# Kernel tuning notes

Hardware: AMD Instinct MI355X
Metric: run time of the kernel (lower is better)

Reference implementation:

```python
import jax, jax.numpy as jnp
import numpy as np

EPS = 1e-5  # BatchNorm eps (PyTorch default)


def gcn_conv(x, edge_index, W, b):
    """PyG GCNConv with add_self_loops=True, normalize=True.
    out[j] = sum_{(i->j)} x_w[i] / sqrt(deg_i * deg_j) + x_w[j] / deg_j + b,
    deg_j = 1 + in-degree(j) (self-loop included)."""
    n = x.shape[0]
    src, dst = edge_index[0], edge_index[1]
    ones = jnp.ones(src.shape[0], x.dtype)
    deg = 1.0 + jax.ops.segment_sum(ones, dst, num_segments=n)  # [n]
    dis = jax.lax.rsqrt(deg)
    xw = x @ W  # [n, out]
    msg = xw[src] * (dis[src] * dis[dst])[:, None]  # gather + per-edge norm
    agg = jax.ops.segment_sum(msg, dst, num_segments=n)  # scatter-add
    agg = agg + xw * (1.0 / deg)[:, None]  # self-loop term
    return agg + b


def bn_relu(x, gamma, beta):
    # BatchNorm1d over the node dim (training-mode batch stats) + ReLU
    mean = x.mean(axis=0)
    var = x.var(axis=0)
    return jax.nn.relu((x - mean) * jax.lax.rsqrt(var + EPS) * gamma + beta)


def wireframe_gnn(x, edge_index, layers, fcW, fcb):
    feats = [x]
    h = x
    for (W, b, g, be) in layers:  # fixed small n_layers loop
        h = bn_relu(gcn_conv(h, edge_index, W, b), g, be)
        feats.append(h)
    cat = jnp.concatenate(feats, axis=1)
    return jax.nn.relu(cat @ fcW + fcb)


N_L, N_J = 50000, 25000
D_FC, NF = 1024, 256
E_L, E_J = 400000, 100000
L_LAB, J_LAB = 10, 3


def setup_inputs() -> dict:
    key = jax.random.key(0)
    ks = iter(jax.random.split(key, 48))
    p = lambda shape: (jax.random.normal(next(ks), shape, jnp.float32) * 0.02)
    inp = {}
    inp["line_features"] = jax.random.normal(next(ks), (N_L, D_FC), jnp.float32)
    inp["junction_features"] = jax.random.normal(next(ks), (N_J, NF), jnp.float32)
    inp["line_edge_index"] = jax.random.randint(next(ks), (2, E_L), 0, N_L, jnp.int64)
    inp["junction_edge_index"] = jax.random.randint(next(ks), (2, E_J), 0, N_J, jnp.int64)
    # line GNN: 1024 -> 512 -> 256, concat 1792 -> fc 1024
    inp["lg_W1"], inp["lg_b1"] = p((D_FC, D_FC // 2)), p((D_FC // 2,))
    inp["lg_g1"], inp["lg_be1"] = jnp.ones(D_FC // 2, jnp.float32), jnp.zeros(D_FC // 2, jnp.float32)
    inp["lg_W2"], inp["lg_b2"] = p((D_FC // 2, D_FC // 4)), p((D_FC // 4,))
    inp["lg_g2"], inp["lg_be2"] = jnp.ones(D_FC // 4, jnp.float32), jnp.zeros(D_FC // 4, jnp.float32)
    cat_l = D_FC + D_FC // 2 + D_FC // 4  # 1792
    inp["lg_fcW"], inp["lg_fcb"] = p((cat_l, D_FC)), p((D_FC,))
    # fc_lines: 1024 -> 1024 -> 1024 -> L_LAB (dim_loi*n_pts1 == dim_fc == 1024)
    inp["fl_W1"], inp["fl_b1"] = p((D_FC, D_FC)), p((D_FC,))
    inp["fl_W2"], inp["fl_b2"] = p((D_FC, D_FC)), p((D_FC,))
    inp["fl_W3"], inp["fl_b3"] = p((D_FC, L_LAB)), p((L_LAB,))
    # junction GNN: 256 -> 128 -> 64, concat 448 -> fc 256
    inp["jg_W1"], inp["jg_b1"] = p((NF, NF // 2)), p((NF // 2,))
    inp["jg_g1"], inp["jg_be1"] = jnp.ones(NF // 2, jnp.float32), jnp.zeros(NF // 2, jnp.float32)
    inp["jg_W2"], inp["jg_b2"] = p((NF // 2, NF // 4)), p((NF // 4,))
    inp["jg_g2"], inp["jg_be2"] = jnp.ones(NF // 4, jnp.float32), jnp.zeros(NF // 4, jnp.float32)
    cat_j = NF + NF // 2 + NF // 4  # 448
    inp["jg_fcW"], inp["jg_fcb"] = p((cat_j, NF)), p((NF,))
    # fc_junction: 256 -> 64 -> J_LAB
    m = NF // 4
    inp["fj_W1"], inp["fj_b1"] = p((NF, m)), p((m,))
    inp["fj_W2"], inp["fj_b2"] = p((m, J_LAB)), p((J_LAB,))
    return inp


def reference(line_features, junction_features, line_edge_index, junction_edge_index,
              lg_W1, lg_b1, lg_g1, lg_be1, lg_W2, lg_b2, lg_g2, lg_be2, lg_fcW, lg_fcb,
              fl_W1, fl_b1, fl_W2, fl_b2, fl_W3, fl_b3,
              jg_W1, jg_b1, jg_g1, jg_be1, jg_W2, jg_b2, jg_g2, jg_be2, jg_fcW, jg_fcb,
              fj_W1, fj_b1, fj_W2, fj_b2):
    # line branch
    h = wireframe_gnn(line_features, line_edge_index,
                      [(lg_W1, lg_b1, lg_g1, lg_be1), (lg_W2, lg_b2, lg_g2, lg_be2)],
                      lg_fcW, lg_fcb)
    h = jax.nn.relu(h @ fl_W1 + fl_b1)
    h = jax.nn.relu(h @ fl_W2 + fl_b2)
    line_logits = h @ fl_W3 + fl_b3
    # junction branch
    g = wireframe_gnn(junction_features, junction_edge_index,
                      [(jg_W1, jg_b1, jg_g1, jg_be1), (jg_W2, jg_b2, jg_g2, jg_be2)],
                      jg_fcW, jg_fcb)
    g = jax.nn.relu(g @ fj_W1 + fj_b1)
    junction_logits = g @ fj_W2 + fj_b2
    return (line_logits, junction_logits)
```

## Files before the change

### kernel.cpp

```cpp
#include <hip/hip_runtime.h>
#include <stdint.h>
#include <stddef.h>

typedef _Float16 f16;
typedef _Float16 f16x8 __attribute__((ext_vector_type(8)));
typedef _Float16 f16x4_t __attribute__((ext_vector_type(4)));
typedef float floatx4 __attribute__((ext_vector_type(4)));

template <int N> struct F16Vec { typedef f16 type __attribute__((ext_vector_type(N))); };

#define BN_EPS 1e-5f

struct WtJob { const float* W; f16* Wt; int K; int N; int tN; int tilebase; };
struct WtBatch { WtJob j[12]; int njobs; int ntiles; };

__global__ void k_wt_tiled(WtBatch b) {
  __shared__ float T[32][33];
  int bt = blockIdx.x;
  int i = 0;
  #pragma unroll 1
  while (i + 1 < b.njobs && bt >= b.j[i + 1].tilebase) ++i;
  WtJob J = b.j[i];
  int t = bt - J.tilebase;
  int tr = t / J.tN, tc = t - tr * J.tN;
  int ty = threadIdx.x >> 5, tx = threadIdx.x & 31;
  #pragma unroll
  for (int s = 0; s < 32; s += 8) {
    int k = tr * 32 + ty + s, n = tc * 32 + tx;
    if (k < J.K && n < J.N) T[ty + s][tx] = J.W[(size_t)k * J.N + n];
  }
  __syncthreads();
  #pragma unroll
  for (int s = 0; s < 32; s += 8) {
    int n = tc * 32 + ty + s, k = tr * 32 + tx;
    if (n < J.N && k < J.K) J.Wt[(size_t)n * J.K + k] = (f16)T[tx][ty + s];
  }
}

__global__ void k_cvt_cols(const float* __restrict__ src, f16* __restrict__ dst,
                           int n, int c, int ldd, int coff) {
  int t = blockIdx.x * blockDim.x + threadIdx.x;
  int cq = c >> 2;
  if (t >= n * cq) return;
  int r = t / cq, j = (t - r * cq) << 2;
  float4 v = *(const float4*)(src + (size_t)r * c + j);
  f16x4_t o; o[0] = (f16)v.x; o[1] = (f16)v.y; o[2] = (f16)v.z; o[3] = (f16)v.w;
  *(f16x4_t*)(dst + (size_t)r * ldd + coff + j) = o;
}

__global__ void k_count2(const int* __restrict__ dL, int EL, int* __restrict__ cntL,
                         const int* __restrict__ dJ, int EJ, int* __restrict__ cntJ) {
  int t = blockIdx.x * blockDim.x + threadIdx.x;
  if (t < EL) atomicAdd(&cntL[dL[t]], 1);
  else if (t < EL + EJ) atomicAdd(&cntJ[dJ[t - EL]], 1);
}

__global__ void k_scan4(const int* __restrict__ cnt, int n, int* __restrict__ rowstart,
                        float* __restrict__ dis) {
  __shared__ int wsum[16];
  __shared__ int carry_s;
  int tid = threadIdx.x, lane = tid & 63, wv = tid >> 6;
  if (tid == 0) { carry_s = 0; rowstart[0] = 0; }
  __syncthreads();
  for (int base = 0; base < n; base += 4096) {
    int i4 = base + tid * 4;
    int4 c = {0, 0, 0, 0};
    if (i4 < n) c = *(const int4*)(cnt + i4);
    int s0 = c.x, s1 = s0 + c.y, s2 = s1 + c.z, s3 = s2 + c.w;
    int x = s3;
    #pragma unroll
    for (int off = 1; off < 64; off <<= 1) {
      int y = __shfl_up(x, off, 64);
      if (lane >= off) x += y;
    }
    if (lane == 63) wsum[wv] = x;
    __syncthreads();
    if (wv == 0) {
      int s = (lane < 16) ? wsum[lane] : 0;
      #pragma unroll
      for (int off = 1; off < 16; off <<= 1) {
        int y = __shfl_up(s, off, 64);
        if (lane >= off) s += y;
      }
      if (lane < 16) wsum[lane] = s;
    }
    __syncthreads();
    int waveoff = (wv == 0) ? 0 : wsum[wv - 1];
    int excl = (x - s3) + waveoff + carry_s;
    if (i4 < n) {
      rowstart[i4 + 1] = excl + s0;
      rowstart[i4 + 2] = excl + s1;
      rowstart[i4 + 3] = excl + s2;
      rowstart[i4 + 4] = excl + s3;
      dis[i4 + 0] = rsqrtf(1.0f + (float)c.x);
      dis[i4 + 1] = rsqrtf(1.0f + (float)c.y);
      dis[i4 + 2] = rsqrtf(1.0f + (float)c.z);
      dis[i4 + 3] = rsqrtf(1.0f + (float)c.w);
    }
    __syncthreads();
    if (tid == 1023) carry_s = excl + s3;
    __syncthreads();
  }
}

__global__ void k_fill2(const int* __restrict__ eiL, int EL, const int* __restrict__ rsL,
                        int* __restrict__ fillL, int* __restrict__ cixL,
                        const int* __restrict__ eiJ, int EJ, const int* __restrict__ rsJ,
                        int* __restrict__ fillJ, int* __restrict__ cixJ) {
  int t = blockIdx.x * blockDim.x + threadIdx.x;
  if (t < EL) {
    int s = eiL[t], d = eiL[EL + t];
    int pos = atomicAdd(&fillL[d], 1);
    cixL[rsL[d] + pos] = s;
  } else if (t < EL + EJ) {
    int u = t - EL;
    int s = eiJ[u], d = eiJ[EJ + u];
    int pos = atomicAdd(&fillJ[d], 1);
    cixJ[rsJ[d] + pos] = s;
  }
}

template <int CPL>
__global__ void k_gather_f16(const f16* __restrict__ xw, int C,
                             const int* __restrict__ rowstart, const int* __restrict__ colidx,
                             const float* __restrict__ dis, const float* __restrict__ bias,
                             f16* __restrict__ dst, int ldd, int coff, int n) {
  typedef typename F16Vec<CPL>::type V;
  int w = threadIdx.x >> 6, l = threadIdx.x & 63;
  int j = blockIdx.x * 4 + w;
  if (j >= n) return;
  float dj = dis[j];
  int rs = rowstart[j], re = rowstart[j + 1];
  int c0 = l * CPL;
  float acc[CPL];
  {
    V p = *(const V*)(xw + (size_t)j * C + c0);
    float s = dj * dj;
    #pragma unroll
    for (int t = 0; t < CPL; ++t) acc[t] = (float)p[t] * s;
  }
  int e = rs;
  for (; e + 2 <= re; e += 2) {
    int s0 = colidx[e], s1 = colidx[e + 1];
    float f0 = dis[s0] * dj, f1 = dis[s1] * dj;
    V p0 = *(const V*)(xw + (size_t)s0 * C + c0);
    V p1 = *(const V*)(xw + (size_t)s1 * C + c0);
    #pragma unroll
    for (int t = 0; t < CPL; ++t) acc[t] += (float)p0[t] * f0 + (float)p1[t] * f1;
  }
  if (e < re) {
    int s0 = colidx[e];
    float f0 = dis[s0] * dj;
    V p0 = *(const V*)(xw + (size_t)s0 * C + c0);
    #pragma unroll
    for (int t = 0; t < CPL; ++t) acc[t] += (float)p0[t] * f0;
  }
  V o;
  #pragma unroll
  for (int t = 0; t < CPL; ++t) o[t] = (f16)(acc[t] + bias[c0 + t]);
  *(V*)(dst + (size_t)j * ldd + coff + c0) = o;
}

__global__ void k_stats(const f16* __restrict__ v, int ldd, int coff, int n, int C,
                        float* __restrict__ sum, float* __restrict__ sumsq) {
  int c = blockIdx.x * blockDim.x + threadIdx.x;
  if (c >= C) return;
  int r0 = blockIdx.y * 128, r1 = min(r0 + 128, n);
  float s = 0.f, s2 = 0.f;
  for (int r = r0; r < r1; ++r) {
    float x = (float)v[(size_t)r * ldd + coff + c];
    s += x; s2 += x * x;
  }
  atomicAdd(&sum[c], s);
  atomicAdd(&sumsq[c], s2);
}

__global__ void k_bnparam(const float* __restrict__ sum, const float* __restrict__ sumsq,
                          const float* __restrict__ gamma, const float* __restrict__ beta,
                          int n, int C, float* __restrict__ scale, float* __restrict__ shift) {
  int c = blockIdx.x * blockDim.x + threadIdx.x;
  if (c >= C) return;
  float mean = sum[c] / (float)n;
  float var = sumsq[c] / (float)n - mean * mean;
  float sc = gamma[c] * rsqrtf(var + BN_EPS);
  scale[c] = sc;
  shift[c] = beta[c] - mean * sc;
}

__global__ void k_bnapply_ip(f16* __restrict__ v, int ldd, int coff, int n, int C,
                             const float* __restrict__ scale, const float* __restrict__ shift) {
  int t = blockIdx.x * blockDim.x + threadIdx.x;
  int cq = C >> 2;
  if (t >= n * cq) return;
  int r = t / cq, c = (t - r * cq) << 2;
  f16* p = v + (size_t)r * ldd + coff + c;
  f16x4_t x = *(f16x4_t*)p;
  float4 sc = *(const float4*)(scale + c);
  float4 sh = *(const float4*)(shift + c);
  f16x4_t o;
  o[0] = (f16)fmaxf((float)x[0] * sc.x + sh.x, 0.f);
  o[1] = (f16)fmaxf((float)x[1] * sc.y + sh.y, 0.f);
  o[2] = (f16)fmaxf((float)x[2] * sc.z + sh.z, 0.f);
  o[3] = (f16)fmaxf((float)x[3] * sc.w + sh.w, 0.f);
  *(f16x4_t*)p = o;
}

__global__ __launch_bounds__(256)
void k_gemm(const f16* __restrict__ A, int lda,
            const f16* __restrict__ Bt,
            void* __restrict__ Cv, int ldc,
            const float* __restrict__ bias, int relu, int outf,
            int M, int N, int K, int mt, int nt, int per) {
  __shared__ f16 Ash[2][128 * 32];
  __shared__ f16 Bsh[2][128 * 32];
  int b = blockIdx.x;
  int g = (b & 7) * per + (b >> 3);
  if (g >= mt * nt) return;
  int tm = (g / nt) * 128, tn = (g % nt) * 128;
  int tid = threadIdx.x, l = tid & 63, w = tid >> 6;

  const f16* ag[2]; const f16* bg[2];
  uint32_t lof[2];
  #pragma unroll
  for (int j = 0; j < 2; ++j) {
    int rl = w * 32 + j * 16 + (l >> 2);
    int ck = l & 3;
    int lc = ck ^ ((rl >> 1) & 3);
    int gr = tm + rl; if (gr > M - 1) gr = M - 1;
    int gn = tn + rl; if (gn > N - 1) gn = N - 1;
    ag[j] = A + (size_t)gr * lda + lc * 8;
    bg[j] = Bt + (size_t)gn * K + lc * 8;
    lof[j] = (uint32_t)(w * 32 + j * 16) * 64;
  }

  int wm = (w >> 1) * 64, wn = (w & 1) * 64;
  int q = l >> 4, l15 = l & 15;
  uint32_t aoffb[4], boffb[4];
  #pragma unroll
  for (int i = 0; i < 4; ++i) {
    int m = wm + i * 16 + l15;
    int n2 = wn + i * 16 + l15;
    aoffb[i] = (uint32_t)(m * 32 + (q ^ ((m >> 1) & 3)) * 8) * 2;
    boffb[i] = (uint32_t)(n2 * 32 + (q ^ ((n2 >> 1) & 3)) * 8) * 2;
  }

  floatx4 acc[4][4];
  #pragma unroll
  for (int i = 0; i < 4; ++i)
    #pragma unroll
    for (int j = 0; j < 4; ++j) acc[i][j] = (floatx4){0.f, 0.f, 0.f, 0.f};

  int nk = K >> 5;
  #pragma unroll
  for (int j = 0; j < 2; ++j) {
    __builtin_amdgcn_global_load_lds(
        (const __attribute__((address_space(1))) void*)ag[j],
        (__attribute__((address_space(3))) void*)((char*)Ash + lof[j]), 16, 0, 0);
    __builtin_amdgcn_global_load_lds(
        (const __attribute__((address_space(1))) void*)bg[j],
        (__attribute__((address_space(3))) void*)((char*)Bsh + lof[j]), 16, 0, 0);
    ag[j] += 32; bg[j] += 32;
  }

  for (int i = 0; i < nk; ++i) {
    __syncthreads();
    if (i + 1 < nk) {
      uint32_t d = ((i + 1) & 1) ? 8192u : 0u;
      #pragma unroll
      for (int j = 0; j < 2; ++j) {
        __builtin_amdgcn_global_load_lds(
            (const __attribute__((address_space(1))) void*)ag[j],
            (__attribute__((address_space(3))) void*)((char*)Ash + d + lof[j]), 16, 0, 0);
        __builtin_amdgcn_global_load_lds(
            (const __attribute__((address_space(1))) void*)bg[j],
            (__attribute__((address_space(3))) void*)((char*)Bsh + d + lof[j]), 16, 0, 0);
        ag[j] += 32; bg[j] += 32;
      }
    }
    uint32_t s = (i & 1) ? 8192u : 0u;
    f16x8 af[4], bf[4];
    #pragma unroll
    for (int ii = 0; ii < 4; ++ii) {
      af[ii] = *(const f16x8*)((const char*)Ash + s + aoffb[ii]);
      bf[ii] = *(const f16x8*)((const char*)Bsh + s + boffb[ii]);
    }
    #pragma unroll
    for (int mi = 0; mi < 4; ++mi)
      #pragma unroll
      for (int ni = 0; ni < 4; ++ni)
        acc[mi][ni] = __builtin_amdgcn_mfma_f32_16x16x32_f16(af[mi], bf[ni], acc[mi][ni], 0, 0, 0);
  }

  #pragma unroll
  for (int ni = 0; ni < 4; ++ni) {
    int col = tn + wn + ni * 16 + l15;
    if (col >= N) continue;
    float bv = bias ? bias[col] : 0.f;
    #pragma unroll
    for (int mi = 0; mi < 4; ++mi) {
      int rowb = tm + wm + mi * 16 + q * 4;
      #pragma unroll
      for (int r = 0; r < 4; ++r) {
        int row = rowb + r;
        if (row < M) {
          float v = acc[mi][ni][r] + bv;
          if (relu) v = fmaxf(v, 0.f);
          if (outf) ((float*)Cv)[(size_t)row * ldc + col] = v;
          else      ((f16*)Cv)[(size_t)row * ldc + col] = (f16)v;
        }
      }
    }
  }
}

#define G_BAR()   __builtin_amdgcn_s_barrier()
#define G_LGKM0() asm volatile("s_waitcnt lgkmcnt(0)" ::: "memory")

#define READ_BF_ALL()                                                         \
  _Pragma("unroll")                                                           \
  for (int ni = 0; ni < 4; ++ni) {                                            \
    bf[ni][0] = *(const f16x8*)(cbp + bbase + ni * 2048 + cof0);              \
    bf[ni][1] = *(const f16x8*)(cbp + bbase + ni * 2048 + cof1);              \
  }

#define READ_AFP(P)                                                           \
  afp[0][0] = *(const f16x8*)(cbp + abase + (2 * (P)) * 2048 + cof0);         \
  afp[0][1] = *(const f16x8*)(cbp + abase + (2 * (P)) * 2048 + cof1);         \
  afp[1][0] = *(const f16x8*)(cbp + abase + (2 * (P) + 1) * 2048 + cof0);     \
  afp[1][1] = *(const f16x8*)(cbp + abase + (2 * (P) + 1) * 2048 + cof1);

#define MFMA_PAIR(P)                                                          \
  __builtin_amdgcn_s_setprio(1);                                              \
  _Pragma("unroll")                                                           \
  for (int ni = 0; ni < 4; ++ni) {                                            \
    acc[2*(P)][ni]   = __builtin_amdgcn_mfma_f32_16x16x32_f16(bf[ni][0], afp[0][0], acc[2*(P)][ni], 0, 0, 0);   \
    acc[2*(P)+1][ni] = __builtin_amdgcn_mfma_f32_16x16x32_f16(bf[ni][0], afp[1][0], acc[2*(P)+1][ni], 0, 0, 0); \
    acc[2*(P)][ni]   = __builtin_amdgcn_mfma_f32_16x16x32_f16(bf[ni][1], afp[0][1], acc[2*(P)][ni], 0, 0, 0);   \
    acc[2*(P)+1][ni] = __builtin_amdgcn_mfma_f32_16x16x32_f16(bf[ni][1], afp[1][1], acc[2*(P)+1][ni], 0, 0, 0); \
  }                                                                           \
  __builtin_amdgcn_s_setprio(0);

__global__ __launch_bounds__(512, 2)
void k_gemm256(const f16* __restrict__ A, int lda,
               const f16* __restrict__ Bt,
               f16* __restrict__ C, int ldc,
               const float* __restrict__ bias, int relu,
               int M, int N, int K, int mt, int nt) {
  __shared__ char lds[131072];
  char* ldsc = (char*)lds;
  int nwg = mt * nt;
  int b = blockIdx.x;
  int xcd = b & 7, lid = b >> 3;
  int q8 = nwg >> 3, r8 = nwg & 7;
  int wg = (xcd < r8 ? xcd * (q8 + 1) : r8 * (q8 + 1) + (xcd - r8) * q8) + lid;
  int tm = (wg / nt) * 256, tn = (wg % nt) * 256;
  int tid = threadIdx.x, l = tid & 63, w = tid >> 6;
  int wm = w >> 2, wn = w & 3;
  int q = l >> 4, l15 = l & 15;
  int nk = K >> 6;

  int r0 = tid >> 3, r1 = r0 + 64;
  int ck = (tid & 7) ^ (r0 & 7);
  int gmA0a = tm + r0;        if (gmA0a > M - 1) gmA0a = M - 1;
  int gmA0b = tm + r1;        if (gmA0b > M - 1) gmA0b = M - 1;
  int gmA1a = tm + 128 + r0;  if (gmA1a > M - 1) gmA1a = M - 1;
  int gmA1b = tm + 128 + r1;  if (gmA1b > M - 1) gmA1b = M - 1;
  int gnB0a = tn + r0;        if (gnB0a > N - 1) gnB0a = N - 1;
  int gnB0b = tn + r1;        if (gnB0b > N - 1) gnB0b = N - 1;
  int gnB1a = tn + 128 + r0;  if (gnB1a > N - 1) gnB1a = N - 1;
  int gnB1b = tn + 128 + r1;  if (gnB1b > N - 1) gnB1b = N - 1;
  const f16* pA0a = A + (size_t)gmA0a * lda + ck * 8;
  const f16* pA0b = A + (size_t)gmA0b * lda + ck * 8;
  const f16* pA1a = A + (size_t)gmA1a * lda + ck * 8;
  const f16* pA1b = A + (size_t)gmA1b * lda + ck * 8;
  const f16* pB0a = Bt + (size_t)gnB0a * K + ck * 8;
  const f16* pB0b = Bt + (size_t)gnB0b * K + ck * 8;
  const f16* pB1a = Bt + (size_t)gnB1a * K + ck * 8;
  const f16* pB1b = Bt + (size_t)gnB1b * K + ck * 8;
  uint32_t dst0 = (uint32_t)tid * 16;

  auto ST2 = [&](const f16*& pa, const f16*& pb, uint32_t dst) {
    __builtin_amdgcn_global_load_lds(
        (const __attribute__((address_space(1))) void*)pa,
        (__attribute__((address_space(3))) void*)(ldsc + dst), 16, 0, 0);
    __builtin_amdgcn_global_load_lds(
        (const __attribute__((address_space(1))) void*)pb,
        (__attribute__((address_space(3))) void*)(ldsc + dst + 8192), 16, 0, 0);
    pa += 64; pb += 64;
  };
  auto SA0 = [&](uint32_t bb) { ST2(pA0a, pA0b, bb + dst0); };
  auto SA1 = [&](uint32_t bb) { ST2(pA1a, pA1b, bb + 16384u + dst0); };
  auto SB0 = [&](uint32_t bb) { ST2(pB0a, pB0b, bb + 32768u + dst0); };
  auto SB1 = [&](uint32_t bb) { ST2(pB1a, pB1b, bb + 49152u + dst0); };

  uint32_t abase = (uint32_t)((wm * 128 + l15) * 128);
  uint32_t bbase = (uint32_t)(32768 + (wn * 64 + l15) * 128);
  uint32_t cof0 = (uint32_t)(((0 + q) ^ (l15 & 7)) * 16);
  uint32_t cof1 = (uint32_t)(((4 + q) ^ (l15 & 7)) * 16);

  floatx4 acc[8][4];
  #pragma unroll
  for (int i = 0; i < 8; ++i)
    #pragma unroll
    for (int j = 0; j < 4; ++j) acc[i][j] = (floatx4){0.f, 0.f, 0.f, 0.f};

  SA0(0u); SA1(0u); SB0(0u); SB1(0u);
  if (nk > 1) { SB0(65536u); SB1(65536u); }

  f16x8 bf[4][2], afp[2][2];
  for (int t = 0; t < nk; ++t) {
    uint32_t cb = (t & 1) ? 65536u : 0u;
    uint32_t ob = 65536u - cb;
    const char* cbp = ldsc + cb;
    if (t + 1 < nk) { asm volatile("s_waitcnt vmcnt(4)" ::: "memory"); }
    else            { asm volatile("s_waitcnt vmcnt(0)" ::: "memory"); }
    G_BAR();
    READ_BF_ALL();
    READ_AFP(0);
    if (t + 1 < nk) SA0(ob);
    G_BAR(); G_LGKM0();
    MFMA_PAIR(0);
    G_BAR();
    READ_AFP(1);
    if (t + 1 < nk) SA1(ob);
    G_BAR(); G_LGKM0();
    MFMA_PAIR(1);
    G_BAR();
    READ_AFP(2);
    if (t + 2 < nk) SB0(cb);
    G_BAR(); G_LGKM0();
    MFMA_PAIR(2);
    G_BAR();
    READ_AFP(3);
    if (t + 2 < nk) SB1(cb);
    G_BAR(); G_LGKM0();
    MFMA_PAIR(3);
  }

  #pragma unroll
  for (int mi = 0; mi < 8; ++mi) {
    int m = tm + wm * 128 + mi * 16 + l15;
    if (m >= M) continue;
    f16* crow = C + (size_t)m * ldc;
    #pragma unroll
    for (int ni = 0; ni < 4; ++ni) {
      int n0 = tn + wn * 64 + ni * 16 + q * 4;
      floatx4 v = acc[mi][ni];
      if (bias) {
        float4 bv = *(const float4*)(bias + n0);
        v[0] += bv.x; v[1] += bv.y; v[2] += bv.z; v[3] += bv.w;
      }
      if (relu) {
        v[0] = fmaxf(v[0], 0.f); v[1] = fmaxf(v[1], 0.f);
        v[2] = fmaxf(v[2], 0.f); v[3] = fmaxf(v[3], 0.f);
      }
      f16x4_t o;
      o[0] = (f16)v[0]; o[1] = (f16)v[1]; o[2] = (f16)v[2]; o[3] = (f16)v[3];
      *(f16x4_t*)(crow + n0) = o;
    }
  }
}

extern "C" void kernel_launch(void* const* d_in, const int* in_sizes, int n_in,
                              void* d_out, int out_size, void* d_ws, size_t ws_size,
                              hipStream_t stream) {
  (void)in_sizes; (void)n_in; (void)out_size; (void)ws_size;
  const int NL = 50000, NJ = 25000, EL = 400000, EJ = 100000;

  const float* x_l  = (const float*)d_in[0];
  const float* x_j  = (const float*)d_in[1];
  const int*   ei_l = (const int*)d_in[2];
  const int*   ei_j = (const int*)d_in[3];
  const float* lgW1 = (const float*)d_in[4];  const float* lgb1 = (const float*)d_in[5];
  const float* lgg1 = (const float*)d_in[6];  const float* lgbe1= (const float*)d_in[7];
  const float* lgW2 = (const float*)d_in[8];  const float* lgb2 = (const float*)d_in[9];
  const float* lgg2 = (const float*)d_in[10]; const float* lgbe2= (const float*)d_in[11];
  const float* lgfcW= (const float*)d_in[12]; const float* lgfcb= (const float*)d_in[13];
  const float* flW1 = (const float*)d_in[14]; const float* flb1 = (const float*)d_in[15];
  const float* flW2 = (const float*)d_in[16]; const float* flb2 = (const float*)d_in[17];
  const float* flW3 = (const float*)d_in[18]; const float* flb3 = (const float*)d_in[19];
  const float* jgW1 = (const float*)d_in[20]; const float* jgb1 = (const float*)d_in[21];
  const float* jgg1 = (const float*)d_in[22]; const float* jgbe1= (const float*)d_in[23];
  const float* jgW2 = (const float*)d_in[24]; const float* jgb2 = (const float*)d_in[25];
  const float* jgg2 = (const float*)d_in[26]; const float* jgbe2= (const float*)d_in[27];
  const float* jgfcW= (const float*)d_in[28]; const float* jgfcb= (const float*)d_in[29];
  const float* fjW1 = (const float*)d_in[30]; const float* fjb1 = (const float*)d_in[31];
  const float* fjW2 = (const float*)d_in[32]; const float* fjb2 = (const float*)d_in[33];

  char* ws = (char*)d_ws;
  size_t off = 0;
  auto alloc = [&](size_t bytes) -> char* {
    char* p = ws + off;
    off += (bytes + 255) & ~(size_t)255;
    return p;
  };

  f16* cat16 = (f16*)alloc((size_t)NL * 1792 * 2);
  f16* hA    = (f16*)alloc((size_t)NL * 1024 * 2);
  f16* hB    = (f16*)alloc((size_t)NL * 1024 * 2);
  f16*  xw16  = (f16*)hB;
  f16* catJ  = (f16*)alloc((size_t)NJ * 448 * 2);
  f16* hJA   = (f16*)alloc((size_t)NJ * 256 * 2);
  f16* hJB   = (f16*)alloc((size_t)NJ * 64 * 2);
  f16*  xwJ   = (f16*)hB;

  f16* W1t   = (f16*)alloc((size_t)1024 * 512 * 2);
  f16* W2t   = (f16*)alloc((size_t)512 * 256 * 2);
  f16* fcWt  = (f16*)alloc((size_t)1792 * 1024 * 2);
  f16* flW1t = (f16*)alloc((size_t)1024 * 1024 * 2);
  f16* flW2t = (f16*)alloc((size_t)1024 * 1024 * 2);
  f16* flW3t = (f16*)alloc((size_t)1024 * 16 * 2);
  f16* jW1t  = (f16*)alloc((size_t)256 * 128 * 2);
  f16* jW2t  = (f16*)alloc((size_t)128 * 64 * 2);
  f16* jfcWt = (f16*)alloc((size_t)448 * 256 * 2);
  f16* fjW1t = (f16*)alloc((size_t)256 * 64 * 2);
  f16* fjW2t = (f16*)alloc((size_t)64 * 4 * 2);

  int* zero0 = (int*)alloc(((size_t)2 * NL + 2 * NJ + 1920) * 4);
  int* cntL  = zero0;
  int* fillL = cntL + NL;
  int* cntJ  = fillL + NL;
  int* fillJ = cntJ + NJ;
  float* stats = (float*)(fillJ + NJ);
  float* sum1L = stats;        float* sq1L = stats + 512;
  float* sum2L = stats + 1024; float* sq2L = stats + 1280;
  float* sum1J = stats + 1536; float* sq1J = stats + 1664;
  float* sum2J = stats + 1792; float* sq2J = stats + 1856;

  int* rsL   = (int*)alloc((size_t)(NL + 4) * 4);
  int* cixL  = (int*)alloc((size_t)EL * 4);
  float* disL= (float*)alloc((size_t)NL * 4);
  int* rsJ   = (int*)alloc((size_t)(NJ + 4) * 4);
  int* cixJ  = (int*)alloc((size_t)EJ * 4);
  float* disJ= (float*)alloc((size_t)NJ * 4);
  float* scalc = (float*)alloc(512 * 4);
  float* shftc = (float*)alloc(512 * 4);

  auto cdiv = [](int a, int b) { return (a + b - 1) / b; };

  auto gemm = [&](const f16* A, int lda, const f16* Bt, void* Cc, int ldc,
                  const float* bias, int relu, int outf, int M, int N, int K) {
    if (!outf && (N & 255) == 0 && N >= 256 && (K & 63) == 0 && K >= 128) {
      int mt = cdiv(M, 256), nt = N >> 8;
      k_gemm256<<<mt * nt, 512, 0, stream>>>(A, lda, Bt, (f16*)Cc, ldc, bias, relu,
                                             M, N, K, mt, nt);
    } else {
      int mt = cdiv(M, 128), nt = cdiv(N, 128);
      int per = cdiv(mt * nt, 8);
      k_gemm<<<8 * per, 256, 0, stream>>>(A, lda, Bt, Cc, ldc, bias, relu, outf,
                                          M, N, K, mt, nt, per);
    }
  };
  auto bn = [&](f16* v, int ldd, int coff, int n, int C,
                float* sum, float* sumsq, const float* gamma, const float* beta) {
    dim3 gs(cdiv(C, 256), cdiv(n, 128));
    k_stats<<<gs, 256, 0, stream>>>(v, ldd, coff, n, C, sum, sumsq);
    k_bnparam<<<cdiv(C, 256), 256, 0, stream>>>(sum, sumsq, gamma, beta, n, C, scalc, shftc);
    k_bnapply_ip<<<cdiv(n * (C >> 2), 256), 256, 0, stream>>>(v, ldd, coff, n, C, scalc, shftc);
  };

  hipMemsetAsync(zero0, 0, ((size_t)2 * NL + 2 * NJ + 1920) * 4, stream);

  {
    WtBatch B2; int base = 0, nj = 0;
    auto add = [&](const float* W, f16* Wt, int K, int N) {
      int tK = cdiv(K, 32), tN = cdiv(N, 32);
      B2.j[nj++] = WtJob{W, Wt, K, N, tN, base};
      base += tK * tN;
    };
    add(lgW1, W1t, 1024, 512);
    add(lgW2, W2t, 512, 256);
    add(lgfcW, fcWt, 1792, 1024);
    add(flW1, flW1t, 1024, 1024);
    add(flW2, flW2t, 1024, 1024);
    add(flW3, flW3t, 1024, 10);
    add(jgW1, jW1t, 256, 128);
    add(jgW2, jW2t, 128, 64);
    add(jgfcW, jfcWt, 448, 256);
    add(fjW1, fjW1t, 256, 64);
    add(fjW2, fjW2t, 64, 3);
    B2.njobs = nj; B2.ntiles = base;
    k_wt_tiled<<<base, 256, 0, stream>>>(B2);
  }

  k_cvt_cols<<<cdiv(NL * 256, 256), 256, 0, stream>>>(x_l, cat16, NL, 1024, 1792, 0);
  k_cvt_cols<<<cdiv(NJ * 64, 256), 256, 0, stream>>>(x_j, catJ, NJ, 256, 448, 0);

  k_count2<<<cdiv(EL + EJ, 256), 256, 0, stream>>>(ei_l + EL, EL, cntL, ei_j + EJ, EJ, cntJ);
  k_scan4<<<1, 1024, 0, stream>>>(cntL, NL, rsL, disL);
  k_scan4<<<1, 1024, 0, stream>>>(cntJ, NJ, rsJ, disJ);
  k_fill2<<<cdiv(EL + EJ, 256), 256, 0, stream>>>(ei_l, EL, rsL, fillL, cixL,
                                                  ei_j, EJ, rsJ, fillJ, cixJ);

  gemm(cat16, 1792, W1t, xw16, 512, nullptr, 0, 0, NL, 512, 1024);
  k_gather_f16<8><<<cdiv(NL, 4), 256, 0, stream>>>(xw16, 512, rsL, cixL, disL, lgb1,
                                                   cat16, 1792, 1024, NL);
  bn(cat16, 1792, 1024, NL, 512, sum1L, sq1L, lgg1, lgbe1);

  gemm(cat16 + 1024, 1792, W2t, xw16, 256, nullptr, 0, 0, NL, 256, 512);
  k_gather_f16<4><<<cdiv(NL, 4), 256, 0, stream>>>(xw16, 256, rsL, cixL, disL, lgb2,
                                                   cat16, 1792, 1536, NL);
  bn(cat16, 1792, 1536, NL, 256, sum2L, sq2L, lgg2, lgbe2);

  gemm(cat16, 1792, fcWt, hA, 1024, lgfcb, 1, 0, NL, 1024, 1792);
  gemm(hA, 1024, flW1t, hB, 1024, flb1, 1, 0, NL, 1024, 1024);
  gemm(hB, 1024, flW2t, hA, 1024, flb2, 1, 0, NL, 1024, 1024);
  gemm(hA, 1024, flW3t, (float*)d_out, 10, flb3, 0, 1, NL, 10, 1024);

  gemm(catJ, 448, jW1t, xwJ, 128, nullptr, 0, 0, NJ, 128, 256);
  k_gather_f16<2><<<cdiv(NJ, 4), 256, 0, stream>>>(xwJ, 128, rsJ, cixJ, disJ, jgb1,
                                                   catJ, 448, 256, NJ);
  bn(catJ, 448, 256, NJ, 128, sum1J, sq1J, jgg1, jgbe1);

  gemm(catJ + 256, 448, jW2t, xwJ, 64, nullptr, 0, 0, NJ, 64, 128);
  k_gather_f16<1><<<cdiv(NJ, 4), 256, 0, stream>>>(xwJ, 64, rsJ, cixJ, disJ, jgb2,
                                                   catJ, 448, 384, NJ);
  bn(catJ, 448, 384, NJ, 64, sum2J, sq2J, jgg2, jgbe2);

  gemm(catJ, 448, jfcWt, hJA, 256, jgfcb, 1, 0, NJ, 256, 448);
  gemm(hJA, 256, fjW1t, hJB, 64, fjb1, 1, 0, NJ, 64, 256);
  gemm(hJB, 64, fjW2t, (float*)d_out + (size_t)NL * 10, 3, fjb2, 0, 1, NJ, 3, 64);
}
```

Baseline: 1.496 ms.

## Reschedule GEMM main loop with fewer barriers and prefetched A fragments

The 256x256 fp16 MFMA GEMM inner loop is rebuilt. Global-to-LDS stores for the next A tile are issued right after the first barrier, and both B stores are grouped after a single mid-loop barrier. The old scheme had four barrier-separated read/compute phases. A fragments for all four sub-steps are now read into separate register arrays, so LDS reads overlap MFMA work, and the s_setprio hints are dropped. The aim is less barrier stalling and better latency hiding, at the cost of many more live vector registers under a 512-thread, 2-block launch bound, which risks spills or lower occupancy.

```diff
diff --git a/kernel.cpp b/kernel.cpp
--- a/kernel.cpp
+++ b/kernel.cpp
@@ -323,22 +323,20 @@
     bf[ni][1] = *(const f16x8*)(cbp + bbase + ni * 2048 + cof1);              \
   }
 
-#define READ_AFP(P)                                                           \
-  afp[0][0] = *(const f16x8*)(cbp + abase + (2 * (P)) * 2048 + cof0);         \
-  afp[0][1] = *(const f16x8*)(cbp + abase + (2 * (P)) * 2048 + cof1);         \
-  afp[1][0] = *(const f16x8*)(cbp + abase + (2 * (P) + 1) * 2048 + cof0);     \
-  afp[1][1] = *(const f16x8*)(cbp + abase + (2 * (P) + 1) * 2048 + cof1);
-
-#define MFMA_PAIR(P)                                                          \
-  __builtin_amdgcn_s_setprio(1);                                              \
+#define READ_AFP(DST, P)                                                      \
+  DST[0] = *(const f16x8*)(cbp + abase + (2 * (P)) * 2048 + cof0);            \
+  DST[1] = *(const f16x8*)(cbp + abase + (2 * (P)) * 2048 + cof1);            \
+  DST[2] = *(const f16x8*)(cbp + abase + (2 * (P) + 1) * 2048 + cof0);        \
+  DST[3] = *(const f16x8*)(cbp + abase + (2 * (P) + 1) * 2048 + cof1);
+
+#define MFMA_PAIR(SRC, P)                                                     \
   _Pragma("unroll")                                                           \
   for (int ni = 0; ni < 4; ++ni) {                                            \
-    acc[2*(P)][ni]   = __builtin_amdgcn_mfma_f32_16x16x32_f16(bf[ni][0], afp[0][0], acc[2*(P)][ni], 0, 0, 0);   \
-    acc[2*(P)+1][ni] = __builtin_amdgcn_mfma_f32_16x16x32_f16(bf[ni][0], afp[1][0], acc[2*(P)+1][ni], 0, 0, 0); \
-    acc[2*(P)][ni]   = __builtin_amdgcn_mfma_f32_16x16x32_f16(bf[ni][1], afp[0][1], acc[2*(P)][ni], 0, 0, 0);   \
-    acc[2*(P)+1][ni] = __builtin_amdgcn_mfma_f32_16x16x32_f16(bf[ni][1], afp[1][1], acc[2*(P)+1][ni], 0, 0, 0); \
-  }                                                                           \
-  __builtin_amdgcn_s_setprio(0);
+    acc[2*(P)][ni]   = __builtin_amdgcn_mfma_f32_16x16x32_f16(bf[ni][0], SRC[0], acc[2*(P)][ni], 0, 0, 0);   \
+    acc[2*(P)+1][ni] = __builtin_amdgcn_mfma_f32_16x16x32_f16(bf[ni][0], SRC[2], acc[2*(P)+1][ni], 0, 0, 0); \
+    acc[2*(P)][ni]   = __builtin_amdgcn_mfma_f32_16x16x32_f16(bf[ni][1], SRC[1], acc[2*(P)][ni], 0, 0, 0);   \
+    acc[2*(P)+1][ni] = __builtin_amdgcn_mfma_f32_16x16x32_f16(bf[ni][1], SRC[3], acc[2*(P)+1][ni], 0, 0, 0); \
+  }
 
 __global__ __launch_bounds__(512, 2)
 void k_gemm256(const f16* __restrict__ A, int lda,
@@ -407,7 +405,7 @@
   SA0(0u); SA1(0u); SB0(0u); SB1(0u);
   if (nk > 1) { SB0(65536u); SB1(65536u); }
 
-  f16x8 bf[4][2], afp[2][2];
+  f16x8 bf[4][2], af0[4], af1[4], af2[4], af3[4];
   for (int t = 0; t < nk; ++t) {
     uint32_t cb = (t & 1) ? 65536u : 0u;
     uint32_t ob = 65536u - cb;
@@ -415,26 +413,20 @@
     if (t + 1 < nk) { asm volatile("s_waitcnt vmcnt(4)" ::: "memory"); }
     else            { asm volatile("s_waitcnt vmcnt(0)" ::: "memory"); }
     G_BAR();
+    __builtin_amdgcn_sched_barrier(0);
+    if (t + 1 < nk) { SA0(ob); SA1(ob); }
     READ_BF_ALL();
-    READ_AFP(0);
-    if (t + 1 < nk) SA0(ob);
-    G_BAR(); G_LGKM0();
-    MFMA_PAIR(0);
+    READ_AFP(af0, 0);
+    READ_AFP(af1, 1);
+    MFMA_PAIR(af0, 0);
+    G_LGKM0();
     G_BAR();
-    READ_AFP(1);
-    if (t + 1 < nk) SA1(ob);
-    G_BAR(); G_LGKM0();
-    MFMA_PAIR(1);
-    G_BAR();
-    READ_AFP(2);
-    if (t + 2 < nk) SB0(cb);
-    G_BAR(); G_LGKM0();
-    MFMA_PAIR(2);
-    G_BAR();
-    READ_AFP(3);
-    if (t + 2 < nk) SB1(cb);
-    G_BAR(); G_LGKM0();
-    MFMA_PAIR(3);
+    if (t + 2 < nk) { SB0(cb); SB1(cb); }
+    READ_AFP(af2, 2);
+    MFMA_PAIR(af1, 1);
+    READ_AFP(af3, 3);
+    MFMA_PAIR(af2, 2);
+    MFMA_PAIR(af3, 3);
   }
 
   #pragma unroll
```

New measurement: 1.449 ms. 3.2% less time.
